# Optimization experiments

Measured on AMD Instinct MI355X. Metric: run time of the kernel, lower is better.

The kernel has to match this reference:

```python
import jax, jax.numpy as jnp
import numpy as np
from jax import lax

C = 256; A = 3; FH = 160; FW = 160
IMG_H = 640.0; IMG_W = 640.0; STRIDE = 4.0; ANCHOR_SIZE = 64.0
OBJ_THR = 0.5; IOU_THR = 0.7; PRE_NMS = 2000; TOP_K = 1000
BN_EPS = 1e-5; NEG = -1e9


def setup_inputs() -> dict:
    key = jax.random.key(0)
    ks = jax.random.split(key, 4)
    s = 0.02
    return {
        "x": jax.random.normal(ks[0], (1, C, FH, FW), jnp.float32),
        "conv_w": jax.random.normal(ks[1], (C, C, 3, 3), jnp.float32) * s,
        "conv_b": jnp.zeros((C,), jnp.float32),
        "bn_gamma": jnp.ones((C,), jnp.float32),
        "bn_beta": jnp.zeros((C,), jnp.float32),
        "bn_mean": jnp.zeros((C,), jnp.float32),
        "bn_var": jnp.ones((C,), jnp.float32),
        "det_w": jax.random.normal(ks[2], (A, C), jnp.float32) * s,
        "det_b": jnp.zeros((A,), jnp.float32),
        "reg_w": jax.random.normal(ks[3], (4 * A, C), jnp.float32) * s,
        "reg_b": jnp.zeros((4 * A,), jnp.float32),
    }


def _make_anchors():
    ars = jnp.array([0.5, 1.0, 2.0], jnp.float32)
    h = ANCHOR_SIZE * jnp.sqrt(ars)
    w = ANCHOR_SIZE / jnp.sqrt(ars)
    base = jnp.stack([-w / 2, -h / 2, w / 2, h / 2], axis=1)  # (A,4)
    sx = jnp.arange(FW, dtype=jnp.float32) * STRIDE
    sy = jnp.arange(FH, dtype=jnp.float32) * STRIDE
    yy, xx = jnp.meshgrid(sy, sx, indexing='ij')  # (FH,FW)
    shifts = jnp.stack([xx, yy, xx, yy], axis=-1)  # (FH,FW,4)
    anchors = base[:, None, None, :] + shifts[None]  # (A,FH,FW,4), anchor-major like RPNHead formatting
    return anchors.reshape(-1, 4)


def _clip(boxes):
    return jnp.stack([
        jnp.clip(boxes[:, 0], 0.0, IMG_W),
        jnp.clip(boxes[:, 1], 0.0, IMG_H),
        jnp.clip(boxes[:, 2], 0.0, IMG_W),
        jnp.clip(boxes[:, 3], 0.0, IMG_H),
    ], axis=1)


def _apply_deltas(boxes, deltas):
    w = boxes[:, 2] - boxes[:, 0]
    h = boxes[:, 3] - boxes[:, 1]
    cx = boxes[:, 0] + 0.5 * w
    cy = boxes[:, 1] + 0.5 * h
    pcx = deltas[:, 0] * w + cx
    pcy = deltas[:, 1] * h + cy
    pw = w * jnp.exp(deltas[:, 2])
    ph = h * jnp.exp(deltas[:, 3])
    return jnp.stack([pcx - 0.5 * pw, pcy - 0.5 * ph, pcx + 0.5 * pw, pcy + 0.5 * ph], axis=1)


def _iou_matrix(b):
    area = (b[:, 2] - b[:, 0]) * (b[:, 3] - b[:, 1])
    lt = jnp.maximum(b[:, None, :2], b[None, :, :2])
    rb = jnp.minimum(b[:, None, 2:], b[None, :, 2:])
    wh = jnp.clip(rb - lt, 0.0)
    inter = wh[..., 0] * wh[..., 1]
    return inter / (area[:, None] + area[None, :] - inter + 1e-9)


def _forward(x, conv_w, conv_b, bn_gamma, bn_beta, bn_mean, bn_var, det_w, det_b, reg_w, reg_b):
    # shared conv + BN(eval) + ReLU
    y = lax.conv_general_dilated(x, conv_w, (1, 1), 'SAME',
                                 dimension_numbers=('NCHW', 'OIHW', 'NCHW')) + conv_b[None, :, None, None]
    scale = bn_gamma / jnp.sqrt(bn_var + BN_EPS)
    y = (y - bn_mean[None, :, None, None]) * scale[None, :, None, None] + bn_beta[None, :, None, None]
    y = jax.nn.relu(y)
    # 1x1 RPN heads
    logits = jnp.einsum('nchw,oc->nohw', y, det_w) + det_b[None, :, None, None]  # (1,A,FH,FW)
    reg = jnp.einsum('nchw,oc->nohw', y, reg_w) + reg_b[None, :, None, None]     # (1,4A,FH,FW)
    # format per RPNHead: (N,1,A,H,W)->permute->(N,A*H*W) and (N,4,A,H,W)->(N,A*H*W,4)
    obj = logits.reshape(1, 1, A, FH, FW).transpose(0, 2, 3, 4, 1).reshape(-1)   # (A*FH*FW,)
    deltas = reg.reshape(1, 4, A, FH, FW).transpose(0, 2, 3, 4, 1).reshape(-1, 4)
    anchors = _clip(_make_anchors())
    proposals = _apply_deltas(anchors, lax.stop_gradient(deltas))
    # _filter_proposals (batch=1)
    lg = lax.stop_gradient(obj)
    props = _clip(proposals)
    score = jax.nn.sigmoid(lg)
    masked = jnp.where(score > OBJ_THR, lg, NEG)  # threshold mask (step 2)
    top_scores, idx = lax.top_k(masked, PRE_NMS)  # pre-NMS top-k (step 3)
    top_boxes = props[idx]
    valid = top_scores > NEG / 2
    iou = _iou_matrix(top_boxes)
    arange = jnp.arange(PRE_NMS)

    def body(i, keep):
        sup = (iou[i] > IOU_THR) & (arange > i)
        return jnp.where(keep[i], keep & ~sup, keep)

    keep = lax.fori_loop(0, PRE_NMS, body, valid)  # greedy NMS (boxes pre-sorted by score)
    rank = jnp.cumsum(keep) - 1
    sel = keep & (rank < TOP_K)
    slot = jnp.where(sel, rank, TOP_K)  # overflow bucket at TOP_K
    filt_logits = jnp.full((TOP_K + 1,), NEG, jnp.float32).at[slot].set(top_scores)[:TOP_K]
    filt_boxes = jnp.zeros((TOP_K + 1, 4), jnp.float32).at[slot].set(top_boxes)[:TOP_K]
    return (anchors, obj, deltas, filt_logits, filt_boxes)


def reference(x, conv_w, conv_b, bn_gamma, bn_beta, bn_mean, bn_var, det_w, det_b, reg_w, reg_b):
    return _forward(x, conv_w, conv_b, bn_gamma, bn_beta, bn_mean, bn_var, det_w, det_b, reg_w, reg_b)
```

## Files before the change

kernel.cpp:

```cpp
#include <hip/hip_runtime.h>
#include <math.h>

#define NPIX  25600
#define NANCH 76800

constexpr int OUT_ANCH = 0;
constexpr int OUT_OBJ  = 307200;
constexpr int OUT_DELT = 384000;
constexpr int OUT_FL   = 691200;
constexpr int OUT_FB   = 692200;

constexpr size_t Y_OFF      = 0;
constexpr size_t PROPS_OFF  = 26214400;
constexpr size_t KEYF_OFF   = PROPS_OFF + 2457600;
constexpr size_t CANDK_OFF  = KEYF_OFF + 307200;
constexpr size_t CANDI_OFF  = CANDK_OFF + 16384;
constexpr size_t TSC_OFF    = CANDI_OFF + 16384;
constexpr size_t TBOX_OFF   = TSC_OFF + 8192;
constexpr size_t HIST_OFF   = TBOX_OFF + 65536;
constexpr size_t STATE_OFF  = HIST_OFF + 1024;
constexpr size_t MASK32_OFF = STATE_OFF + 256;

struct SelState { unsigned prefix; int remaining; int cntHi; int cntEq; };

__device__ __forceinline__ unsigned orderKey32(float f) {
  unsigned u = __float_as_uint(f);
  return (u & 0x80000000u) ? ~u : (u | 0x80000000u);
}
__device__ __forceinline__ float key32ToFloat(unsigned k) {
  unsigned u = (k & 0x80000000u) ? (k & 0x7fffffffu) : ~k;
  return __uint_as_float(u);
}

__global__ __launch_bounds__(256) void prep_all(const float* __restrict__ w,
                                                float* __restrict__ wt,
                                                const float* __restrict__ det_w,
                                                const float* __restrict__ reg_w,
                                                float* __restrict__ wt2,
                                                float* __restrict__ out,
                                                unsigned* __restrict__ hist,
                                                SelState* __restrict__ st) {
  int gid = blockIdx.x * 256 + threadIdx.x;
  int oc  = gid / 2304;
  int rem = gid - oc * 2304;
  int ci  = rem / 9;
  int t   = rem - ci * 9;
  wt[((size_t)ci * 256 + oc) * 9 + t] = w[gid];
  if (gid < 4096) {
    int c = gid >> 4, j = gid & 15;
    float v = 0.f;
    if (j < 3) v = det_w[j * 256 + c];
    else if (j < 15) v = reg_w[(j - 3) * 256 + c];
    wt2[gid] = v;
  }
  if (gid < 1000) out[OUT_FL + gid] = -1e9f;
  if (gid < 4000) out[OUT_FB + gid] = 0.f;
  if (gid < 256) hist[gid] = 0u;
  if (gid == 0) { st->prefix = 0u; st->remaining = 2000; st->cntHi = 0; st->cntEq = 0; }
}

__global__ __launch_bounds__(256) void conv_hyb_f32r(
    const float* __restrict__ x, const float* __restrict__ wt,
    const float* __restrict__ bv, const float* __restrict__ gamma,
    const float* __restrict__ beta, const float* __restrict__ mean,
    const float* __restrict__ var, float* __restrict__ y) {
  const int tile = blockIdx.x;
  const int th0 = (tile / 10) * 16;
  const int tw0 = (tile - (tile / 10) * 10) * 16;
  const int ob  = blockIdx.y * 32;
  const int tid = threadIdx.x;
  const int wid  = __builtin_amdgcn_readfirstlane(tid >> 6);
  const int lane = tid & 63;
  const int r  = lane >> 2;
  const int cg = lane & 3;
  const int oc0 = ob + wid * 8;

  __shared__ __align__(16) float lin[8][18][20];

  float sreg[11];
  auto loadRegs = [&](int cb) {
#pragma unroll
    for (int k = 0; k < 11; ++k) {
      int idx = tid + k * 256;
      float v = 0.f;
      if (idx < 2592) {
        int ci = idx / 324; int rem = idx - ci * 324;
        int rr = rem / 18;  int cc = rem - rr * 18;
        int gh = th0 + rr - 1, gw = tw0 + cc - 1;
        if ((unsigned)gh < 160u && (unsigned)gw < 160u)
          v = x[(size_t)(cb + ci) * NPIX + gh * 160 + gw];
      }
      sreg[k] = v;
    }
  };
  auto writeRegs = [&]() {
#pragma unroll
    for (int k = 0; k < 11; ++k) {
      int idx = tid + k * 256;
      if (idx < 2592) {
        int ci = idx / 324; int rem = idx - ci * 324;
        int rr = rem / 18;  int cc = rem - rr * 18;
        lin[ci][rr][cc] = sreg[k];
      }
    }
  };

  float acc[8][4];
#pragma unroll
  for (int o = 0; o < 8; ++o)
#pragma unroll
    for (int j = 0; j < 4; ++j) acc[o][j] = 0.f;

  loadRegs(248);
  for (int cb = 248; cb >= 0; cb -= 8) {
    __syncthreads();
    writeRegs();
    __syncthreads();
    if (cb > 0) loadRegs(cb - 8);
#pragma unroll
    for (int ci = 7; ci >= 0; --ci) {
      float in0[6], in1[6], in2[6];
      const float* base = &lin[ci][r][cg * 4];
      {
        float4 q = *(const float4*)(base);
        float2 p = *(const float2*)(base + 4);
        in0[0] = q.x; in0[1] = q.y; in0[2] = q.z; in0[3] = q.w; in0[4] = p.x; in0[5] = p.y;
      }
      {
        float4 q = *(const float4*)(base + 20);
        float2 p = *(const float2*)(base + 24);
        in1[0] = q.x; in1[1] = q.y; in1[2] = q.z; in1[3] = q.w; in1[4] = p.x; in1[5] = p.y;
      }
      {
        float4 q = *(const float4*)(base + 40);
        float2 p = *(const float2*)(base + 44);
        in2[0] = q.x; in2[1] = q.y; in2[2] = q.z; in2[3] = q.w; in2[4] = p.x; in2[5] = p.y;
      }
      const float* wb = wt + ((size_t)(cb + ci) * 256 + oc0) * 9;
#pragma unroll
      for (int o = 0; o < 8; ++o) {
        const float w0 = wb[o * 9 + 0], w1 = wb[o * 9 + 1], w2 = wb[o * 9 + 2];
        const float w3 = wb[o * 9 + 3], w4 = wb[o * 9 + 4], w5 = wb[o * 9 + 5];
        const float w6 = wb[o * 9 + 6], w7 = wb[o * 9 + 7], w8 = wb[o * 9 + 8];
#pragma unroll
        for (int j = 0; j < 4; ++j) {
          float a = acc[o][j];
          a = fmaf(in2[j + 2], w8, a); a = fmaf(in2[j + 1], w7, a); a = fmaf(in2[j + 0], w6, a);
          a = fmaf(in1[j + 2], w5, a); a = fmaf(in1[j + 1], w4, a); a = fmaf(in1[j + 0], w3, a);
          a = fmaf(in0[j + 2], w2, a); a = fmaf(in0[j + 1], w1, a); a = fmaf(in0[j + 0], w0, a);
          acc[o][j] = a;
        }
      }
    }
  }

  const int gh = th0 + r, gw0 = tw0 + cg * 4;
#pragma unroll
  for (int o = 0; o < 8; ++o) {
    int oc = oc0 + o;
    float sc = gamma[oc] / sqrtf(var[oc] + 1e-5f);
    float sh = (bv[oc] - mean[oc]) * sc + beta[oc];
    float4 vv;
    float v0 = fmaf(acc[o][0], sc, sh); vv.x = (v0 > 0.f) ? v0 : 0.f;
    float v1 = fmaf(acc[o][1], sc, sh); vv.y = (v1 > 0.f) ? v1 : 0.f;
    float v2 = fmaf(acc[o][2], sc, sh); vv.z = (v2 > 0.f) ? v2 : 0.f;
    float v3 = fmaf(acc[o][3], sc, sh); vv.w = (v3 > 0.f) ? v3 : 0.f;
    *(float4*)&y[(size_t)oc * NPIX + gh * 160 + gw0] = vv;
  }
}

__global__ __launch_bounds__(64) void heads_kernel(
    const float* __restrict__ y, const float* __restrict__ wt2,
    const float* __restrict__ det_b, const float* __restrict__ reg_b,
    float* __restrict__ out, double* __restrict__ props,
    float* __restrict__ keyf) {
  const int p = blockIdx.x * 64 + threadIdx.x;
  float od0 = 0.f, od1 = 0.f, od2 = 0.f;
  float rg[12];
#pragma unroll
  for (int o = 0; o < 12; ++o) rg[o] = 0.f;
  const float* yp = y + p;
  for (int c = 255; c >= 0; --c) {
    float v = yp[(size_t)c * NPIX];
    const float* wc = wt2 + c * 16;
    od0 = fmaf(v, wc[0], od0);
    od1 = fmaf(v, wc[1], od1);
    od2 = fmaf(v, wc[2], od2);
#pragma unroll
    for (int o = 0; o < 12; ++o) rg[o] = fmaf(v, wc[3 + o], rg[o]);
  }
  const int hh = p / 160;
  const int ww = p - hh * 160;
  const float sx = ww * 4.0f, sy = hh * 4.0f;
  float odv[3] = {od0, od1, od2};
#pragma unroll
  for (int a = 0; a < 3; ++a) {
    float ar = (a == 0) ? 0.5f : ((a == 1) ? 1.0f : 2.0f);
    float sq = sqrtf(ar);
    float haf = 64.0f * sq, waf = 64.0f / sq;
    float ax1 = fminf(fmaxf(sx - waf * 0.5f, 0.f), 640.f);
    float ay1 = fminf(fmaxf(sy - haf * 0.5f, 0.f), 640.f);
    float ax2 = fminf(fmaxf(sx + waf * 0.5f, 0.f), 640.f);
    float ay2 = fminf(fmaxf(sy + haf * 0.5f, 0.f), 640.f);
    int ai = a * NPIX + p;
    out[OUT_ANCH + ai * 4 + 0] = ax1;
    out[OUT_ANCH + ai * 4 + 1] = ay1;
    out[OUT_ANCH + ai * 4 + 2] = ax2;
    out[OUT_ANCH + ai * 4 + 3] = ay2;
    float logit = odv[a] + det_b[a];
    out[OUT_OBJ + ai] = logit;
    float dx = rg[0 + a] + reg_b[0 + a];
    float dy = rg[3 + a] + reg_b[3 + a];
    float dw = rg[6 + a] + reg_b[6 + a];
    float dh = rg[9 + a] + reg_b[9 + a];
    out[OUT_DELT + ai * 4 + 0] = dx;
    out[OUT_DELT + ai * 4 + 1] = dy;
    out[OUT_DELT + ai * 4 + 2] = dw;
    out[OUT_DELT + ai * 4 + 3] = dh;
    float aw = ax2 - ax1, ah = ay2 - ay1;
    float cx = ax1 + 0.5f * aw, cy = ay1 + 0.5f * ah;
    float pcx = dx * aw + cx, pcy = dy * ah + cy;
    float pw = aw * expf(dw), ph = ah * expf(dh);
    props[ai * 4 + 0] = (double)fminf(fmaxf(pcx - 0.5f * pw, 0.f), 640.f);
    props[ai * 4 + 1] = (double)fminf(fmaxf(pcy - 0.5f * ph, 0.f), 640.f);
    props[ai * 4 + 2] = (double)fminf(fmaxf(pcx + 0.5f * pw, 0.f), 640.f);
    props[ai * 4 + 3] = (double)fminf(fmaxf(pcy + 0.5f * ph, 0.f), 640.f);
    keyf[ai] = (logit > 0.f) ? logit : -1e9f;
  }
}

__global__ __launch_bounds__(256) void hist_pass(const float* __restrict__ keyf,
                                                 unsigned* __restrict__ hist,
                                                 const SelState* __restrict__ st, int pass) {
  __shared__ unsigned lh[256];
  lh[threadIdx.x] = 0u;
  __syncthreads();
  unsigned prefix = st->prefix;
  int shift = 24 - 8 * pass;
  int i = blockIdx.x * 256 + threadIdx.x;
  unsigned k = orderKey32(keyf[i]);
  bool ok = (pass == 0) || ((k >> (shift + 8)) == prefix);
  if (ok) atomicAdd(&lh[(k >> shift) & 255u], 1u);
  __syncthreads();
  unsigned c = lh[threadIdx.x];
  if (c) atomicAdd(&hist[threadIdx.x], c);
}

__global__ __launch_bounds__(64) void pick_kernel(unsigned* __restrict__ hist,
                                                  SelState* __restrict__ st) {
  const int lane = threadIdx.x;
  const int rem = st->remaining;
  unsigned h0 = hist[lane * 4 + 0], h1 = hist[lane * 4 + 1];
  unsigned h2 = hist[lane * 4 + 2], h3 = hist[lane * 4 + 3];
  unsigned lsum = h0 + h1 + h2 + h3;
  unsigned acc = lsum;
#pragma unroll
  for (int off = 1; off < 64; off <<= 1) {
    unsigned other = (unsigned)__shfl_down((int)acc, off);
    if (lane + off < 64) acc += other;
  }
  unsigned long long m = __ballot(acc >= (unsigned)rem);
  int L = 63 - __clzll(m);
  if (lane == L) {
    unsigned tail = acc - lsum;
    unsigned s3 = h3 + tail, s2 = h2 + s3, s1 = h1 + s2, s0 = h0 + s1;
    int b; unsigned suf, hsel;
    if (s3 >= (unsigned)rem)      { b = lane * 4 + 3; suf = s3; hsel = h3; }
    else if (s2 >= (unsigned)rem) { b = lane * 4 + 2; suf = s2; hsel = h2; }
    else if (s1 >= (unsigned)rem) { b = lane * 4 + 1; suf = s1; hsel = h1; }
    else                          { b = lane * 4 + 0; suf = s0; hsel = h0; }
    st->prefix = (st->prefix << 8) | (unsigned)b;
    st->remaining = rem - (int)(suf - hsel);
  }
  hist[lane * 4 + 0] = 0u; hist[lane * 4 + 1] = 0u;
  hist[lane * 4 + 2] = 0u; hist[lane * 4 + 3] = 0u;
}

__global__ __launch_bounds__(256) void compact_kernel(const float* __restrict__ keyf,
                                                      SelState* __restrict__ st,
                                                      unsigned* __restrict__ candk,
                                                      unsigned* __restrict__ candi) {
  int i = blockIdx.x * 256 + threadIdx.x;
  if (i >= NANCH) return;
  unsigned k = orderKey32(keyf[i]);
  unsigned T = st->prefix;
  if (k > T) {
    int pos = atomicAdd(&st->cntHi, 1);
    if (pos < 2048) { candk[pos] = k; candi[pos] = (unsigned)i; }
  } else if (k == T) {
    int pos = atomicAdd(&st->cntEq, 1);
    if (pos < 2048) { candk[2048 + pos] = k; candi[2048 + pos] = (unsigned)i; }
  }
}

__global__ __launch_bounds__(1024) void sort_gather(const unsigned* __restrict__ candk,
                                                    const unsigned* __restrict__ candi,
                                                    const SelState* __restrict__ st,
                                                    const double* __restrict__ props,
                                                    float* __restrict__ tsc,
                                                    double* __restrict__ tbox) {
  __shared__ unsigned ka[4096];
  __shared__ unsigned ia[4096];
  int nHi = st->cntHi; if (nHi > 2048) nHi = 2048;
  int nEq = st->cntEq; if (nEq > 2048) nEq = 2048;
  for (int i = threadIdx.x; i < 4096; i += 1024) {
    bool real = (i < nHi) || (i >= 2048 && i < 2048 + nEq);
    ka[i] = real ? candk[i] : 0u;
    ia[i] = real ? candi[i] : 0xffffffffu;
  }
  __syncthreads();
  for (int k = 2; k <= 4096; k <<= 1) {
    for (int j = k >> 1; j > 0; j >>= 1) {
      for (int e = threadIdx.x; e < 4096; e += 1024) {
        int l = e ^ j;
        if (l > e) {
          unsigned ke = ka[e], kl = ka[l];
          unsigned ie = ia[e], il = ia[l];
          bool descending = ((e & k) == 0);
          bool lBetter = (kl > ke) || (kl == ke && il < ie);
          bool eBetter = (ke > kl) || (ke == kl && ie < il);
          bool sw = descending ? lBetter : eBetter;
          if (sw) { ka[e] = kl; ka[l] = ke; ia[e] = il; ia[l] = ie; }
        }
      }
      __syncthreads();
    }
  }
  for (int t = threadIdx.x; t < 2000; t += 1024) {
    unsigned idx = ia[t];
    if (idx < (unsigned)NANCH) {
      tsc[t] = key32ToFloat(ka[t]);
      tbox[t * 4 + 0] = props[(size_t)idx * 4 + 0];
      tbox[t * 4 + 1] = props[(size_t)idx * 4 + 1];
      tbox[t * 4 + 2] = props[(size_t)idx * 4 + 2];
      tbox[t * 4 + 3] = props[(size_t)idx * 4 + 3];
    } else {
      tsc[t] = -1e9f;
      tbox[t * 4 + 0] = 0.0; tbox[t * 4 + 1] = 0.0;
      tbox[t * 4 + 2] = 0.0; tbox[t * 4 + 3] = 0.0;
    }
  }
}

__global__ __launch_bounds__(256) void iou_mask(const double* __restrict__ tbox,
                                                unsigned* __restrict__ mask32) {
  int gid = blockIdx.x * 256 + threadIdx.x;
  if (gid >= 2000 * 64) return;
  int i = gid >> 6, l = gid & 63;
  int j0 = l * 32;
  unsigned m = 0u;
  if (j0 + 31 > i) {
    double bix = tbox[i * 4 + 0], biy = tbox[i * 4 + 1];
    double biz = tbox[i * 4 + 2], biw = tbox[i * 4 + 3];
    double areai = (biz - bix) * (biw - biy);
#pragma unroll 4
    for (int b = 0; b < 32; ++b) {
      int j = j0 + b;
      if (j >= 2000 || j <= i) continue;
      double bjx = tbox[j * 4 + 0], bjy = tbox[j * 4 + 1];
      double bjz = tbox[j * 4 + 2], bjw = tbox[j * 4 + 3];
      double xx1 = fmax(bix, bjx), yy1 = fmax(biy, bjy);
      double xx2 = fmin(biz, bjz), yy2 = fmin(biw, bjw);
      double iw = fmax(xx2 - xx1, 0.0), ih = fmax(yy2 - yy1, 0.0);
      double inter = iw * ih;
      double areaj = (bjz - bjx) * (bjw - bjy);
      double iou = inter / (areai + areaj - inter + 1e-9);
      if (iou > 0.7) m |= (1u << b);
    }
  }
  mask32[(size_t)i * 64 + l] = m;
}

__global__ __launch_bounds__(64) void nms_scan(const unsigned* __restrict__ mask32,
                                               const float* __restrict__ tsc,
                                               const double* __restrict__ tbox,
                                               float* __restrict__ out) {
  __shared__ unsigned kw[64];
  __shared__ unsigned wpfx[65];
  __shared__ __align__(16) unsigned stage[2][2048];
  const int lane = threadIdx.x;

  kw[lane] = 0u;
  for (int i = lane; i < 2000; i += 64)
    if (tsc[i] > -5e8f) atomicOr(&kw[i >> 5], 1u << (i & 31));
  const unsigned Vw = kw[lane];
  unsigned S = 0u;

  uint4 s0, s1, s2, s3, s4, s5, s6, s7;
  int nchunks = 0;
  auto stageLoad = [&](int w) {
    int rows = 2000 - w * 32; if (rows > 32) rows = 32;
    nchunks = rows >> 2;
    const uint4* src = (const uint4*)(mask32 + (size_t)w * 2048);
    if (nchunks > 0) s0 = src[0 * 64 + lane];
    if (nchunks > 1) s1 = src[1 * 64 + lane];
    if (nchunks > 2) s2 = src[2 * 64 + lane];
    if (nchunks > 3) s3 = src[3 * 64 + lane];
    if (nchunks > 4) s4 = src[4 * 64 + lane];
    if (nchunks > 5) s5 = src[5 * 64 + lane];
    if (nchunks > 6) s6 = src[6 * 64 + lane];
    if (nchunks > 7) s7 = src[7 * 64 + lane];
  };
  auto stageWrite = [&](int buf) {
    uint4* dst = (uint4*)&stage[buf][0];
    if (nchunks > 0) dst[0 * 64 + lane] = s0;
    if (nchunks > 1) dst[1 * 64 + lane] = s1;
    if (nchunks > 2) dst[2 * 64 + lane] = s2;
    if (nchunks > 3) dst[3 * 64 + lane] = s3;
    if (nchunks > 4) dst[4 * 64 + lane] = s4;
    if (nchunks > 5) dst[5 * 64 + lane] = s5;
    if (nchunks > 6) dst[6 * 64 + lane] = s6;
    if (nchunks > 7) dst[7 * 64 + lane] = s7;
  };

  stageLoad(0);
  stageWrite(0);
  for (int w = 0; w < 63; ++w) {
    const int buf = w & 1;
    if (w + 1 < 63) stageLoad(w + 1);
    unsigned rem = (unsigned)__shfl((int)(Vw & ~S), w);
    while (rem) {
      int b = __ffs(rem) - 1;
      rem &= rem - 1;
      unsigned mlane = stage[buf][b * 64 + lane];
      unsigned supw  = stage[buf][b * 64 + w];
      S |= mlane;
      rem &= ~supw;
    }
    if (w + 1 < 63) stageWrite(buf ^ 1);
  }
  kw[lane] = Vw & ~S;

  if (lane == 0) {
    wpfx[0] = 0;
    for (int w = 0; w < 64; ++w) wpfx[w + 1] = wpfx[w] + __popc(kw[w]);
  }
  for (int i = lane; i < 2000; i += 64) {
    if ((kw[i >> 5] >> (i & 31)) & 1u) {
      int r = (int)wpfx[i >> 5] + __popc(kw[i >> 5] & ((1u << (i & 31)) - 1u));
      if (r < 1000) {
        out[OUT_FL + r] = tsc[i];
        out[OUT_FB + r * 4 + 0] = (float)tbox[i * 4 + 0];
        out[OUT_FB + r * 4 + 1] = (float)tbox[i * 4 + 1];
        out[OUT_FB + r * 4 + 2] = (float)tbox[i * 4 + 2];
        out[OUT_FB + r * 4 + 3] = (float)tbox[i * 4 + 3];
      }
    }
  }
}

extern "C" void kernel_launch(void* const* d_in, const int* in_sizes, int n_in,
                              void* d_out, int out_size, void* d_ws, size_t ws_size,
                              hipStream_t stream) {
  (void)in_sizes; (void)n_in; (void)out_size; (void)ws_size;
  const float* x      = (const float*)d_in[0];
  const float* conv_w = (const float*)d_in[1];
  const float* conv_b = (const float*)d_in[2];
  const float* gamma  = (const float*)d_in[3];
  const float* beta   = (const float*)d_in[4];
  const float* mean   = (const float*)d_in[5];
  const float* var    = (const float*)d_in[6];
  const float* det_w  = (const float*)d_in[7];
  const float* det_b  = (const float*)d_in[8];
  const float* reg_w  = (const float*)d_in[9];
  const float* reg_b  = (const float*)d_in[10];
  float* out = (float*)d_out;
  char* ws = (char*)d_ws;

  float*  y      = (float*)(ws + Y_OFF);
  double* props  = (double*)(ws + PROPS_OFF);
  float*  wt     = (float*)(ws + PROPS_OFF);
  float*  keyf   = (float*)(ws + KEYF_OFF);
  unsigned* candk = (unsigned*)(ws + CANDK_OFF);
  unsigned* candi = (unsigned*)(ws + CANDI_OFF);
  float*  tsc    = (float*)(ws + TSC_OFF);
  double* tbox   = (double*)(ws + TBOX_OFF);
  unsigned* hist = (unsigned*)(ws + HIST_OFF);
  SelState* st   = (SelState*)(ws + STATE_OFF);
  unsigned* mask32 = (unsigned*)(ws + MASK32_OFF);
  float*  wt2    = (float*)(ws + MASK32_OFF);

  prep_all<<<2304, 256, 0, stream>>>(conv_w, wt, det_w, reg_w, wt2, out, hist, st);
  conv_hyb_f32r<<<dim3(100, 8), 256, 0, stream>>>(x, wt, conv_b, gamma, beta, mean, var, y);
  heads_kernel<<<400, 64, 0, stream>>>(y, wt2, det_b, reg_b, out, props, keyf);
  for (int p = 0; p < 4; ++p) {
    hist_pass<<<300, 256, 0, stream>>>(keyf, hist, st, p);
    pick_kernel<<<1, 64, 0, stream>>>(hist, st);
  }
  compact_kernel<<<300, 256, 0, stream>>>(keyf, st, candk, candi);
  sort_gather<<<1, 1024, 0, stream>>>(candk, candi, st, props, tsc, tbox);
  iou_mask<<<500, 256, 0, stream>>>(tbox, mask32);
  nms_scan<<<1, 64, 0, stream>>>(mask32, tsc, tbox, out);
}
```

Before: 913.7 us.

## Replace four-pass 8-bit radix select with single 16-bit histogram pass

The top-k threshold search drops its four histogram-plus-pick kernel pairs. It now builds one 65536-bin histogram over the upper 16 key bits, filled with global atomics and cleared inside the heads kernel. A single pick kernel finds the threshold bucket, and compaction compares the upper 16 bits instead of the full key. This removes six launches and three passes over the keys. In exchange it uses global atomic contention, and the equal bucket can now hold many keys that may overflow the 2048-slot candidate buffer.

```diff
diff --git a/kernel.cpp b/kernel.cpp
--- a/kernel.cpp
+++ b/kernel.cpp
@@ -38,7 +38,6 @@
                                                 const float* __restrict__ reg_w,
                                                 float* __restrict__ wt2,
                                                 float* __restrict__ out,
-                                                unsigned* __restrict__ hist,
                                                 SelState* __restrict__ st) {
   int gid = blockIdx.x * 256 + threadIdx.x;
   int oc  = gid / 2304;
@@ -55,7 +54,6 @@
   }
   if (gid < 1000) out[OUT_FL + gid] = -1e9f;
   if (gid < 4000) out[OUT_FB + gid] = 0.f;
-  if (gid < 256) hist[gid] = 0u;
   if (gid == 0) { st->prefix = 0u; st->remaining = 2000; st->cntHi = 0; st->cntEq = 0; }
 }
 
@@ -173,8 +171,10 @@
     const float* __restrict__ y, const float* __restrict__ wt2,
     const float* __restrict__ det_b, const float* __restrict__ reg_b,
     float* __restrict__ out, double* __restrict__ props,
-    float* __restrict__ keyf) {
+    float* __restrict__ keyf, unsigned* __restrict__ h16) {
   const int p = blockIdx.x * 64 + threadIdx.x;
+  h16[p] = 0u; h16[p + 25600] = 0u;
+  if (p + 51200 < 65536) h16[p + 51200] = 0u;
   float od0 = 0.f, od1 = 0.f, od2 = 0.f;
   float rg[12];
 #pragma unroll
@@ -229,51 +229,43 @@
   }
 }
 
-__global__ __launch_bounds__(256) void hist_pass(const float* __restrict__ keyf,
-                                                 unsigned* __restrict__ hist,
-                                                 const SelState* __restrict__ st, int pass) {
-  __shared__ unsigned lh[256];
-  lh[threadIdx.x] = 0u;
+__global__ __launch_bounds__(256) void hist16_kernel(const float* __restrict__ keyf,
+                                                     unsigned* __restrict__ h16) {
+  int i = blockIdx.x * 256 + threadIdx.x;
+  float kf = keyf[i];
+  if (kf > -5e8f) atomicAdd(&h16[orderKey32(kf) >> 16], 1u);
+}
+
+__global__ __launch_bounds__(256) void pick16_kernel(const unsigned* __restrict__ h16,
+                                                     SelState* __restrict__ st) {
+  __shared__ unsigned suf[256];
+  const int t = threadIdx.x;
+  const uint4* hp = (const uint4*)(h16 + t * 256);
+  unsigned csum = 0;
+#pragma unroll
+  for (int q = 0; q < 64; ++q) { uint4 v = hp[q]; csum += v.x + v.y + v.z + v.w; }
+  suf[t] = csum;
   __syncthreads();
-  unsigned prefix = st->prefix;
-  int shift = 24 - 8 * pass;
-  int i = blockIdx.x * 256 + threadIdx.x;
-  unsigned k = orderKey32(keyf[i]);
-  bool ok = (pass == 0) || ((k >> (shift + 8)) == prefix);
-  if (ok) atomicAdd(&lh[(k >> shift) & 255u], 1u);
+  if (t == 0) {
+    unsigned run = 0;
+    for (int i = 255; i >= 0; --i) { run += suf[i]; suf[i] = run; }
+  }
   __syncthreads();
-  unsigned c = lh[threadIdx.x];
-  if (c) atomicAdd(&hist[threadIdx.x], c);
-}
-
-__global__ __launch_bounds__(64) void pick_kernel(unsigned* __restrict__ hist,
-                                                  SelState* __restrict__ st) {
-  const int lane = threadIdx.x;
-  const int rem = st->remaining;
-  unsigned h0 = hist[lane * 4 + 0], h1 = hist[lane * 4 + 1];
-  unsigned h2 = hist[lane * 4 + 2], h3 = hist[lane * 4 + 3];
-  unsigned lsum = h0 + h1 + h2 + h3;
-  unsigned acc = lsum;
-#pragma unroll
-  for (int off = 1; off < 64; off <<= 1) {
-    unsigned other = (unsigned)__shfl_down((int)acc, off);
-    if (lane + off < 64) acc += other;
-  }
-  unsigned long long m = __ballot(acc >= (unsigned)rem);
-  int L = 63 - __clzll(m);
-  if (lane == L) {
-    unsigned tail = acc - lsum;
-    unsigned s3 = h3 + tail, s2 = h2 + s3, s1 = h1 + s2, s0 = h0 + s1;
-    int b; unsigned suf, hsel;
-    if (s3 >= (unsigned)rem)      { b = lane * 4 + 3; suf = s3; hsel = h3; }
-    else if (s2 >= (unsigned)rem) { b = lane * 4 + 2; suf = s2; hsel = h2; }
-    else if (s1 >= (unsigned)rem) { b = lane * 4 + 1; suf = s1; hsel = h1; }
-    else                          { b = lane * 4 + 0; suf = s0; hsel = h0; }
-    st->prefix = (st->prefix << 8) | (unsigned)b;
-    st->remaining = rem - (int)(suf - hsel);
-  }
-  hist[lane * 4 + 0] = 0u; hist[lane * 4 + 1] = 0u;
-  hist[lane * 4 + 2] = 0u; hist[lane * 4 + 3] = 0u;
+  unsigned mine  = suf[t];
+  unsigned above = (t == 255) ? 0u : suf[t + 1];
+  if (mine >= 2000u && above < 2000u) {
+    unsigned run = above; int B = t * 256;
+    for (int b = 255; b >= 0; --b) {
+      run += h16[t * 256 + b];
+      if (run >= 2000u) { B = t * 256 + b; break; }
+    }
+    st->prefix = (unsigned)B;
+    st->cntHi = 0; st->cntEq = 0;
+  }
+  if (t == 0 && suf[0] < 2000u) {
+    st->prefix = orderKey32(-1e9f) >> 16;
+    st->cntHi = 0; st->cntEq = 0;
+  }
 }
 
 __global__ __launch_bounds__(256) void compact_kernel(const float* __restrict__ keyf,
@@ -283,11 +275,12 @@
   int i = blockIdx.x * 256 + threadIdx.x;
   if (i >= NANCH) return;
   unsigned k = orderKey32(keyf[i]);
-  unsigned T = st->prefix;
-  if (k > T) {
+  unsigned B = st->prefix;
+  unsigned h = k >> 16;
+  if (h > B) {
     int pos = atomicAdd(&st->cntHi, 1);
     if (pos < 2048) { candk[pos] = k; candi[pos] = (unsigned)i; }
-  } else if (k == T) {
+  } else if (h == B) {
     int pos = atomicAdd(&st->cntEq, 1);
     if (pos < 2048) { candk[2048 + pos] = k; candi[2048 + pos] = (unsigned)i; }
   }
@@ -475,18 +468,16 @@
   unsigned* candi = (unsigned*)(ws + CANDI_OFF);
   float*  tsc    = (float*)(ws + TSC_OFF);
   double* tbox   = (double*)(ws + TBOX_OFF);
-  unsigned* hist = (unsigned*)(ws + HIST_OFF);
   SelState* st   = (SelState*)(ws + STATE_OFF);
   unsigned* mask32 = (unsigned*)(ws + MASK32_OFF);
   float*  wt2    = (float*)(ws + MASK32_OFF);
-
-  prep_all<<<2304, 256, 0, stream>>>(conv_w, wt, det_w, reg_w, wt2, out, hist, st);
+  unsigned* h16  = (unsigned*)(ws + MASK32_OFF + 16384);
+
+  prep_all<<<2304, 256, 0, stream>>>(conv_w, wt, det_w, reg_w, wt2, out, st);
   conv_hyb_f32r<<<dim3(100, 8), 256, 0, stream>>>(x, wt, conv_b, gamma, beta, mean, var, y);
-  heads_kernel<<<400, 64, 0, stream>>>(y, wt2, det_b, reg_b, out, props, keyf);
-  for (int p = 0; p < 4; ++p) {
-    hist_pass<<<300, 256, 0, stream>>>(keyf, hist, st, p);
-    pick_kernel<<<1, 64, 0, stream>>>(hist, st);
-  }
+  heads_kernel<<<400, 64, 0, stream>>>(y, wt2, det_b, reg_b, out, props, keyf, h16);
+  hist16_kernel<<<300, 256, 0, stream>>>(keyf, h16);
+  pick16_kernel<<<1, 256, 0, stream>>>(h16, st);
   compact_kernel<<<300, 256, 0, stream>>>(keyf, st, candk, candi);
   sort_gather<<<1, 1024, 0, stream>>>(candk, candi, st, props, tsc, tbox);
   iou_mask<<<500, 256, 0, stream>>>(tbox, mask32);
```

Result: slower. 932.3 us (+2.0%).
